# Optimization experiments

Measured on AMD Instinct MI355X. Metric: run time of the kernel, lower is better.

The kernel has to match this reference:

```python
import jax, jax.numpy as jnp
import numpy as np

B, C, H, W = 8, 19, 512, 1024
IGNORE_LABEL = -1


def setup_inputs() -> dict:
    key = jax.random.key(0)
    k1, k2, k3 = jax.random.split(key, 3)
    logits = jax.random.normal(k1, (B, C, H, W), dtype=jnp.float32)
    labels = jax.random.randint(k2, (B, H, W), 0, C, dtype=jnp.int32)
    # smooth_labels: per-pixel class probability distribution [B, C, H, W]
    smooth_labels = jax.nn.softmax(jax.random.normal(k3, (B, C, H, W), dtype=jnp.float32), axis=1)
    return {"logits": logits, "labels": labels, "smooth_labels": smooth_labels}


def reference(logits, labels, smooth_labels):
    # nn.CrossEntropyLoss(ignore_index=IGNORE_LABEL, reduction='none'):
    # per-pixel NLL of log-softmax over class dim, 0 at ignored pixels.
    num_classes = logits.shape[1]
    logp = jax.nn.log_softmax(logits, axis=1)                       # [B,C,H,W]
    safe_labels = jnp.clip(labels, 0, num_classes - 1)
    nll = -jnp.take_along_axis(logp, safe_labels[:, None], axis=1)[:, 0]  # [B,H,W]
    valid = labels != IGNORE_LABEL
    pixel_losses = jnp.where(valid, nll, 0.0)
    # Original module returns pixel_losses.mean() over ALL pixels (ignored
    # pixels contribute 0 to the numerator but ARE counted in the mean's
    # denominator, matching reduction='none' followed by .mean()).
    # The OHEM branch (smooth-label CE, gather, sort, threshold) computes
    # pixel_losses_2 but the result is discarded in the source forward.
    return pixel_losses.mean()
```

## Files before the change

kernel.cpp:

```cpp
#include <hip/hip_runtime.h>

#define BB   8
#define CC   19
#define HH   512
#define WW   1024
#define HWSZ (HH * WW)
#define NPIX ((long long)BB * HWSZ)
#define BLOCK 256
#define PIX_PER_THREAD 4
#define NQUAD (NPIX / PIX_PER_THREAD)
#define GRID  ((int)(NQUAD / BLOCK))

__global__ __launch_bounds__(BLOCK) void ce_partial_kernel(
        const float* __restrict__ logits,
        const int*   __restrict__ labels,
        float*       __restrict__ partial) {
    long long q = (long long)blockIdx.x * BLOCK + threadIdx.x;
    long long p = q * PIX_PER_THREAD;
    int b  = (int)(p / HWSZ);
    int hw = (int)(p - (long long)b * HWSZ);
    const float* base = logits + (long long)b * CC * HWSZ + hw;

    float a[PIX_PER_THREAD][CC];
#pragma unroll
    for (int c = 0; c < CC; ++c) {
        float4 t = *reinterpret_cast<const float4*>(base + (long long)c * HWSZ);
        a[0][c] = t.x; a[1][c] = t.y; a[2][c] = t.z; a[3][c] = t.w;
    }
    int4 lab4 = *reinterpret_cast<const int4*>(labels + p);
    int labv[PIX_PER_THREAD] = { lab4.x, lab4.y, lab4.z, lab4.w };

    float local = 0.0f;
#pragma unroll
    for (int j = 0; j < PIX_PER_THREAD; ++j) {
        float m = a[j][0];
#pragma unroll
        for (int c = 1; c < CC; ++c) m = fmaxf(m, a[j][c]);
        float s = 0.0f;
        float pick = 0.0f;
#pragma unroll
        for (int c = 0; c < CC; ++c) {
            s += __expf(a[j][c] - m);
            pick = (labv[j] == c) ? a[j][c] : pick;
        }
        float nll = m + __logf(s) - pick;
        local += (labv[j] != -1) ? nll : 0.0f;
    }

#pragma unroll
    for (int off = 32; off > 0; off >>= 1)
        local += __shfl_down(local, off);

    __shared__ float smem[BLOCK / 64];
    int wave = threadIdx.x >> 6;
    int lane = threadIdx.x & 63;
    if (lane == 0) smem[wave] = local;
    __syncthreads();
    if (threadIdx.x == 0) {
        float bs = 0.0f;
#pragma unroll
        for (int w = 0; w < BLOCK / 64; ++w) bs += smem[w];
        partial[blockIdx.x] = bs;
    }
}

__global__ __launch_bounds__(256) void ce_final_kernel(
        const float* __restrict__ partial,
        float*       __restrict__ out) {
    double s = 0.0;
    for (int i = threadIdx.x; i < GRID; i += 256)
        s += (double)partial[i];
#pragma unroll
    for (int off = 32; off > 0; off >>= 1)
        s += __shfl_down(s, off);

    __shared__ double smem[4];
    int wave = threadIdx.x >> 6;
    int lane = threadIdx.x & 63;
    if (lane == 0) smem[wave] = s;
    __syncthreads();
    if (threadIdx.x == 0) {
        double tot = smem[0] + smem[1] + smem[2] + smem[3];
        out[0] = (float)(tot / (double)NPIX);
    }
}

extern "C" void kernel_launch(void* const* d_in, const int* in_sizes, int n_in,
                              void* d_out, int out_size, void* d_ws, size_t ws_size,
                              hipStream_t stream) {
    const float* logits = (const float*)d_in[0];
    const int*   labels = (const int*)d_in[1];
    float* out     = (float*)d_out;
    float* partial = (float*)d_ws;

    ce_partial_kernel<<<GRID, BLOCK, 0, stream>>>(logits, labels, partial);
    ce_final_kernel<<<1, 256, 0, stream>>>(partial, out);
}
```

Measured before the change: 69.30 us.

## Split class loop into two chunks with online softmax merge and nontemporal loads

The partial kernel now loads the 19 class channels in two chunks of 10 and 9 and reduces each chunk separately, then merges the two max/sum pairs with an online-softmax rescale. This cuts peak register use (fewer live floats), which may raise occupancy. All logits and label loads become nontemporal vector loads, and index math uses shifts instead of division. The final kernel uses 1024 threads that each read one float4, which assumes GRID equals exactly 4096. It costs two extra exps per pixel and splits the loads into two separate batches.

```diff
diff --git a/kernel.cpp b/kernel.cpp
--- a/kernel.cpp
+++ b/kernel.cpp
@@ -1,50 +1,87 @@
 #include <hip/hip_runtime.h>
 
-#define BB   8
-#define CC   19
-#define HH   512
-#define WW   1024
-#define HWSZ (HH * WW)
-#define NPIX ((long long)BB * HWSZ)
+#define CC    19
+#define HWSH  19
+#define HWSZ  (512 * 1024)
+#define NPIX  (8LL * HWSZ)
 #define BLOCK 256
-#define PIX_PER_THREAD 4
-#define NQUAD (NPIX / PIX_PER_THREAD)
-#define GRID  ((int)(NQUAD / BLOCK))
+#define PPT   4
+#define GRID  ((int)(NPIX / PPT / BLOCK))
+
+typedef float f32x4 __attribute__((ext_vector_type(4)));
+typedef int   i32x4 __attribute__((ext_vector_type(4)));
+
+__device__ __forceinline__ f32x4 ntload_f4(const float* p) {
+    return __builtin_nontemporal_load(reinterpret_cast<const f32x4*>(p));
+}
+__device__ __forceinline__ i32x4 ntload_i4(const int* p) {
+    return __builtin_nontemporal_load(reinterpret_cast<const i32x4*>(p));
+}
+
+template <int N>
+__device__ __forceinline__ void chunk_reduce(const float (&a)[N], int lab,
+                                             int c0, float& m, float& s,
+                                             float& pick) {
+    m = a[0];
+#pragma unroll
+    for (int c = 1; c < N; ++c) m = fmaxf(m, a[c]);
+    s = 0.0f;
+#pragma unroll
+    for (int c = 0; c < N; ++c) {
+        s += __expf(a[c] - m);
+        pick = (lab == c0 + c) ? a[c] : pick;
+    }
+}
 
 __global__ __launch_bounds__(BLOCK) void ce_partial_kernel(
         const float* __restrict__ logits,
         const int*   __restrict__ labels,
         float*       __restrict__ partial) {
     long long q = (long long)blockIdx.x * BLOCK + threadIdx.x;
-    long long p = q * PIX_PER_THREAD;
-    int b  = (int)(p / HWSZ);
-    int hw = (int)(p - (long long)b * HWSZ);
-    const float* base = logits + (long long)b * CC * HWSZ + hw;
+    long long p = q * PPT;
+    int b  = (int)(p >> HWSH);
+    int hw = (int)(p & (HWSZ - 1));
+    const float* base = logits + ((long long)b * CC << HWSH) + hw;
 
-    float a[PIX_PER_THREAD][CC];
-#pragma unroll
-    for (int c = 0; c < CC; ++c) {
-        float4 t = *reinterpret_cast<const float4*>(base + (long long)c * HWSZ);
-        a[0][c] = t.x; a[1][c] = t.y; a[2][c] = t.z; a[3][c] = t.w;
-    }
-    int4 lab4 = *reinterpret_cast<const int4*>(labels + p);
-    int labv[PIX_PER_THREAD] = { lab4.x, lab4.y, lab4.z, lab4.w };
+    i32x4 lab4 = ntload_i4(labels + p);
+    int labv[PPT] = { lab4.x, lab4.y, lab4.z, lab4.w };
 
     float local = 0.0f;
+
+    float m1[PPT], s1[PPT], pick[PPT] = {0, 0, 0, 0};
+    {
+        float a0[10], a1[10], a2[10], a3[10];
 #pragma unroll
-    for (int j = 0; j < PIX_PER_THREAD; ++j) {
-        float m = a[j][0];
+        for (int c = 0; c < 10; ++c) {
+            f32x4 t = ntload_f4(base + ((long long)c << HWSH));
+            a0[c] = t.x; a1[c] = t.y; a2[c] = t.z; a3[c] = t.w;
+        }
+        chunk_reduce(a0, labv[0], 0, m1[0], s1[0], pick[0]);
+        chunk_reduce(a1, labv[1], 0, m1[1], s1[1], pick[1]);
+        chunk_reduce(a2, labv[2], 0, m1[2], s1[2], pick[2]);
+        chunk_reduce(a3, labv[3], 0, m1[3], s1[3], pick[3]);
+    }
+
+    {
+        float a0[9], a1[9], a2[9], a3[9];
 #pragma unroll
-        for (int c = 1; c < CC; ++c) m = fmaxf(m, a[j][c]);
-        float s = 0.0f;
-        float pick = 0.0f;
+        for (int c = 0; c < 9; ++c) {
+            f32x4 t = ntload_f4(base + ((long long)(c + 10) << HWSH));
+            a0[c] = t.x; a1[c] = t.y; a2[c] = t.z; a3[c] = t.w;
+        }
+        float m2[PPT], s2[PPT];
+        chunk_reduce(a0, labv[0], 10, m2[0], s2[0], pick[0]);
+        chunk_reduce(a1, labv[1], 10, m2[1], s2[1], pick[1]);
+        chunk_reduce(a2, labv[2], 10, m2[2], s2[2], pick[2]);
+        chunk_reduce(a3, labv[3], 10, m2[3], s2[3], pick[3]);
+
 #pragma unroll
-        for (int c = 0; c < CC; ++c) {
-            s += __expf(a[j][c] - m);
-            pick = (labv[j] == c) ? a[j][c] : pick;
+        for (int j = 0; j < PPT; ++j) {
+            float mm = fmaxf(m1[j], m2[j]);
+            float ss = s1[j] * __expf(m1[j] - mm) + s2[j] * __expf(m2[j] - mm);
+            float nll = mm + __logf(ss) - pick[j];
+            local += (labv[j] != -1) ? nll : 0.0f;
         }
-        float nll = m + __logf(s) - pick;
-        local += (labv[j] != -1) ? nll : 0.0f;
     }
 
 #pragma unroll
@@ -52,9 +89,7 @@
         local += __shfl_down(local, off);
 
     __shared__ float smem[BLOCK / 64];
-    int wave = threadIdx.x >> 6;
-    int lane = threadIdx.x & 63;
-    if (lane == 0) smem[wave] = local;
+    if ((threadIdx.x & 63) == 0) smem[threadIdx.x >> 6] = local;
     __syncthreads();
     if (threadIdx.x == 0) {
         float bs = 0.0f;
@@ -64,23 +99,22 @@
     }
 }
 
-__global__ __launch_bounds__(256) void ce_final_kernel(
+__global__ __launch_bounds__(1024) void ce_final_kernel(
         const float* __restrict__ partial,
         float*       __restrict__ out) {
-    double s = 0.0;
-    for (int i = threadIdx.x; i < GRID; i += 256)
-        s += (double)partial[i];
+    f32x4 v = *reinterpret_cast<const f32x4*>(partial + threadIdx.x * 4);
+    double s = (double)v.x + (double)v.y + (double)v.z + (double)v.w;
 #pragma unroll
     for (int off = 32; off > 0; off >>= 1)
         s += __shfl_down(s, off);
 
-    __shared__ double smem[4];
-    int wave = threadIdx.x >> 6;
-    int lane = threadIdx.x & 63;
-    if (lane == 0) smem[wave] = s;
+    __shared__ double smem[16];
+    if ((threadIdx.x & 63) == 0) smem[threadIdx.x >> 6] = s;
     __syncthreads();
     if (threadIdx.x == 0) {
-        double tot = smem[0] + smem[1] + smem[2] + smem[3];
+        double tot = 0.0;
+#pragma unroll
+        for (int w = 0; w < 16; ++w) tot += smem[w];
         out[0] = (float)(tot / (double)NPIX);
     }
 }
@@ -94,5 +128,5 @@
     float* partial = (float*)d_ws;
 
     ce_partial_kernel<<<GRID, BLOCK, 0, stream>>>(logits, labels, partial);
-    ce_final_kernel<<<1, 256, 0, stream>>>(partial, out);
+    ce_final_kernel<<<1, 1024, 0, stream>>>(partial, out);
 }
```

Measured after the change: 58.47 us (median of 2 runs). 1.19x faster.
